# Kernel tuning notes

Measured on AMD Instinct MI355X. Metric: run time of the kernel, lower is better.

The kernel has to match this reference:

```python
import jax, jax.numpy as jnp
import numpy as np

UNITS = 32
SENSORY = 16
MOTOR = 3
ODE_UNFOLDS = 3
EPS = 1e-8


def setup_inputs() -> dict:
    key = jax.random.key(0)
    ks = jax.random.split(key, 16)
    B, T, D = 64, 512, 6
    return {
        "x": jax.random.normal(ks[0], (B, T, D), jnp.float32),
        "mean_us": jax.random.normal(ks[1], (1, 1, D), jnp.float32),
        "std_us": jnp.ones((1, 1, D), jnp.float32),
        "pre_w1": jax.random.normal(ks[2], (D, 32), jnp.float32) * 0.4,
        "pre_b1": jnp.zeros((32,), jnp.float32),
        "pre_w2": jax.random.normal(ks[3], (32, SENSORY), jnp.float32) * 0.18,
        "pre_b2": jnp.zeros((SENSORY,), jnp.float32),
        "input_w": jnp.ones((SENSORY,), jnp.float32),
        "input_b": jnp.zeros((SENSORY,), jnp.float32),
        "sensory_mu": jax.random.uniform(ks[4], (SENSORY, UNITS), jnp.float32),
        "sensory_sigma": jax.random.uniform(ks[5], (SENSORY, UNITS), jnp.float32),
        "sensory_w": jax.random.uniform(ks[6], (SENSORY, UNITS), jnp.float32),
        "sensory_erev": jax.random.normal(ks[7], (SENSORY, UNITS), jnp.float32),
        "mu": jax.random.uniform(ks[8], (UNITS, UNITS), jnp.float32),
        "sigma": jax.random.uniform(ks[9], (UNITS, UNITS), jnp.float32),
        "w": jax.random.uniform(ks[10], (UNITS, UNITS), jnp.float32),
        "erev": jax.random.normal(ks[11], (UNITS, UNITS), jnp.float32),
        "gleak": jax.random.uniform(ks[12], (UNITS,), jnp.float32),
        "vleak": jax.random.normal(ks[13], (UNITS,), jnp.float32),
        "cm": jax.random.uniform(ks[14], (UNITS,), jnp.float32) + 0.1,
        "output_w": jnp.ones((MOTOR,), jnp.float32),
        "output_b": jnp.zeros((MOTOR,), jnp.float32),
    }


def reference(x, mean_us, std_us, pre_w1, pre_b1, pre_w2, pre_b2,
              input_w, input_b, sensory_mu, sensory_sigma, sensory_w,
              sensory_erev, mu, sigma, w, erev, gleak, vleak, cm,
              output_w, output_b):
    B = x.shape[0]
    # normalize (broadcast of [1,1,6] stats == expand_as in torch)
    xn = (x - mean_us) / std_us
    # DgaPreNet: per-timestep MLP 6 -> 32 -> 16
    feat = jax.nn.gelu(jnp.einsum("btd,dh->bth", xn, pre_w1) + pre_b1)
    feat = jnp.einsum("bth,hs->bts", feat, pre_w2) + pre_b2  # [B,T,S]
    # LTC input mapping
    feat = feat * input_w + input_b
    # sensory synapse activations, precomputed for all timesteps
    s_act = sensory_w * jax.nn.sigmoid(sensory_sigma * (feat[..., None] - sensory_mu))  # [B,T,S,U]
    w_num_sens = jnp.einsum("btsu,su->btu", s_act, sensory_erev)  # [B,T,U]
    w_den_sens = s_act.sum(axis=2)                                # [B,T,U]
    cm_t = cm * ODE_UNFOLDS  # cm / (elapsed_time=1 / ode_unfolds)

    def step(v, inp):
        wns, wds = inp  # [B,U] each
        for _ in range(ODE_UNFOLDS):
            act = w * jax.nn.sigmoid(sigma * (v[:, :, None] - mu))  # [B,U_pre,U_post]
            w_num = jnp.einsum("bpu,pu->bu", act, erev) + wns
            w_den = act.sum(axis=1) + wds
            v = (cm_t * v + gleak * vleak + w_num) / (cm_t + gleak + w_den + EPS)
        out = v[:, :MOTOR] * output_w + output_b
        return v, out

    v0 = jnp.zeros((B, UNITS), x.dtype)
    _, outs = jax.lax.scan(step, v0,
                           (jnp.swapaxes(w_num_sens, 0, 1), jnp.swapaxes(w_den_sens, 0, 1)))
    outs = jnp.swapaxes(outs, 0, 1)  # [B,T,3]
    return outs * std_us[:, :, 0:MOTOR] + mean_us[:, :, 0:MOTOR]
```

## Files before the change

### kernel.cpp

```cpp
#include <hip/hip_runtime.h>

#define T_LEN 512
#define BATCH 64
#define LOG2E 1.4426950408889634f

typedef float v2f __attribute__((ext_vector_type(2)));

#if defined(__has_builtin)
#  if __has_builtin(__builtin_amdgcn_exp2f)
#    define EXP2F(x) __builtin_amdgcn_exp2f(x)
#  endif
#endif
#ifndef EXP2F
#  define EXP2F(x) __expf((x) * 0.6931471805599453f)
#endif

__device__ __forceinline__ float fast_sigmoid(float x) {
    return __builtin_amdgcn_rcpf(1.0f + __expf(-x));
}

__global__ __launch_bounds__(256, 1) void sensory_precompute_kernel(
    const float* __restrict__ x,
    const float* __restrict__ mean_us,
    const float* __restrict__ std_us,
    const float* __restrict__ pre_w1,
    const float* __restrict__ pre_b1,
    const float* __restrict__ pre_w2,
    const float* __restrict__ pre_b2,
    const float* __restrict__ input_w,
    const float* __restrict__ input_b,
    const float* __restrict__ s_mu,
    const float* __restrict__ s_sigma,
    const float* __restrict__ s_w,
    const float* __restrict__ s_erev,
    float* __restrict__ wnd_out,
    int total)
{
    const int idx = blockIdx.x * blockDim.x + threadIdx.x;
    if (idx >= total) return;

    const float* xp = x + (size_t)idx * 6;
    float xn[6];
    #pragma unroll
    for (int d = 0; d < 6; ++d)
        xn[d] = (xp[d] - mean_us[d]) / std_us[d];

    float f1[32];
    #pragma unroll
    for (int h = 0; h < 32; ++h) {
        float a = pre_b1[h];
        #pragma unroll
        for (int d = 0; d < 6; ++d)
            a = fmaf(xn[d], pre_w1[d * 32 + h], a);
        const float y2 = 1.5957691216057308f * fmaf(0.044715f * a * a, a, a);
        f1[h] = a * fast_sigmoid(y2);
    }

    float wn[32], wd[32];
    #pragma unroll
    for (int u = 0; u < 32; ++u) { wn[u] = 0.0f; wd[u] = 0.0f; }

    for (int s = 0; s < 16; ++s) {
        float a = pre_b2[s];
        #pragma unroll
        for (int h = 0; h < 32; ++h)
            a = fmaf(f1[h], pre_w2[h * 16 + s], a);
        const float fs = fmaf(a, input_w[s], input_b[s]);
        #pragma unroll
        for (int u = 0; u < 32; ++u) {
            const int o = s * 32 + u;
            const float sact =
                s_w[o] * fast_sigmoid(s_sigma[o] * (fs - s_mu[o]));
            wn[u] = fmaf(sact, s_erev[o], wn[u]);
            wd[u] += sact;
        }
    }

    float* wo = wnd_out + (size_t)idx * 64;
    #pragma unroll
    for (int u = 0; u < 32; ++u) {
        wo[u * 2]     = wn[u];
        wo[u * 2 + 1] = wd[u];
    }
}

__global__ __launch_bounds__(64, 1) void ltc_scan_kernel(
    const float* __restrict__ wnd_all,
    const float* __restrict__ mu,
    const float* __restrict__ sigma,
    const float* __restrict__ w,
    const float* __restrict__ erev,
    const float* __restrict__ gleak,
    const float* __restrict__ vleak,
    const float* __restrict__ cm,
    const float* __restrict__ output_w,
    const float* __restrict__ output_b,
    const float* __restrict__ mean_us,
    const float* __restrict__ std_us,
    float* __restrict__ out)
{
    const int b = blockIdx.x;
    const int lane = threadIdx.x;
    const int u = lane & 31;
    const int pbase = (lane >> 5) << 4;

    __shared__ float vbuf[64];

    v2f A2[8], B2[8], W2[8], WE2[8];
    #pragma unroll
    for (int i = 0; i < 16; ++i) {
        const int o = (pbase + i) * 32 + u;
        const float sg = sigma[o];
        const float ww = w[o];
        A2[i >> 1][i & 1]  = -sg * LOG2E;
        B2[i >> 1][i & 1]  = sg * mu[o] * LOG2E;
        W2[i >> 1][i & 1]  = ww;
        WE2[i >> 1][i & 1] = ww * erev[o];
    }
    const float cmt  = cm[u] * 3.0f;
    const float gl   = gleak[u];
    const float glvl = gl * vleak[u];

    float osc = 0.0f, osh = 0.0f;
    if (lane < 3) {
        const float sd = std_us[lane];
        osc = output_w[lane] * sd;
        osh = fmaf(output_b[lane], sd, mean_us[lane]);
    }

    const float* wnd_b = wnd_all + (size_t)b * T_LEN * 64 + u * 2;
    float* out_b = out + ((size_t)b * T_LEN) * 3;

    float v = 0.0f;
    vbuf[lane] = 0.0f;
    float2 wnd = *(const float2*)wnd_b;

    for (int t = 0; t < T_LEN; ++t) {
        float2 wnd_n = make_float2(0.0f, 0.0f);
        if (t + 1 < T_LEN)
            wnd_n = *(const float2*)(wnd_b + (size_t)(t + 1) * 64);

        #pragma unroll
        for (int k = 0; k < 3; ++k) {
            const float4* vb = (const float4*)(vbuf + pbase);
            const float4 q0 = vb[0], q1 = vb[1], q2 = vb[2], q3 = vb[3];
            v2f vp[8];
            vp[0] = (v2f){q0.x, q0.y}; vp[1] = (v2f){q0.z, q0.w};
            vp[2] = (v2f){q1.x, q1.y}; vp[3] = (v2f){q1.z, q1.w};
            vp[4] = (v2f){q2.x, q2.y}; vp[5] = (v2f){q2.z, q2.w};
            vp[6] = (v2f){q3.x, q3.y}; vp[7] = (v2f){q3.z, q3.w};

            v2f wna = (v2f){0.f, 0.f}, wnb = (v2f){0.f, 0.f};
            v2f wda = (v2f){0.f, 0.f}, wdb = (v2f){0.f, 0.f};
            #pragma unroll
            for (int j = 0; j < 8; ++j) {
                const v2f arg = A2[j] * vp[j] + B2[j];
                v2f e;
                e.x = EXP2F(arg.x);
                e.y = EXP2F(arg.y);
                const v2f d = e + 1.0f;
                v2f s;
                s.x = __builtin_amdgcn_rcpf(d.x);
                s.y = __builtin_amdgcn_rcpf(d.y);
                if (j & 1) { wnb = WE2[j] * s + wnb; wdb = W2[j] * s + wdb; }
                else       { wna = WE2[j] * s + wna; wda = W2[j] * s + wda; }
            }
            const v2f wn2 = wna + wnb;
            const v2f wd2 = wda + wdb;
            float wnum = wn2.x + wn2.y;
            float wden = wd2.x + wd2.y;
            wnum += __shfl_xor(wnum, 32, 64);
            wden += __shfl_xor(wden, 32, 64);

            const float num = fmaf(cmt, v, glvl + wnum + wnd.x);
            const float den = cmt + gl + wden + wnd.y + 1e-8f;
            v = num * __builtin_amdgcn_rcpf(den);
            vbuf[lane] = v;
        }

        if (lane < 3)
            out_b[t * 3 + lane] = fmaf(v, osc, osh);

        wnd = wnd_n;
    }
}

extern "C" void kernel_launch(void* const* d_in, const int* in_sizes, int n_in,
                              void* d_out, int out_size, void* d_ws, size_t ws_size,
                              hipStream_t stream) {
    const float* x        = (const float*)d_in[0];
    const float* mean_us  = (const float*)d_in[1];
    const float* std_us   = (const float*)d_in[2];
    const float* pre_w1   = (const float*)d_in[3];
    const float* pre_b1   = (const float*)d_in[4];
    const float* pre_w2   = (const float*)d_in[5];
    const float* pre_b2   = (const float*)d_in[6];
    const float* input_w  = (const float*)d_in[7];
    const float* input_b  = (const float*)d_in[8];
    const float* s_mu     = (const float*)d_in[9];
    const float* s_sigma  = (const float*)d_in[10];
    const float* s_w      = (const float*)d_in[11];
    const float* s_erev   = (const float*)d_in[12];
    const float* mu       = (const float*)d_in[13];
    const float* sigma    = (const float*)d_in[14];
    const float* w        = (const float*)d_in[15];
    const float* erev     = (const float*)d_in[16];
    const float* gleak    = (const float*)d_in[17];
    const float* vleak    = (const float*)d_in[18];
    const float* cm       = (const float*)d_in[19];
    const float* output_w = (const float*)d_in[20];
    const float* output_b = (const float*)d_in[21];

    const int total = BATCH * T_LEN;

    float* wnd = (float*)d_ws;

    sensory_precompute_kernel<<<(total + 255) / 256, 256, 0, stream>>>(
        x, mean_us, std_us, pre_w1, pre_b1, pre_w2, pre_b2,
        input_w, input_b, s_mu, s_sigma, s_w, s_erev,
        wnd, total);

    ltc_scan_kernel<<<BATCH, 64, 0, stream>>>(
        wnd, mu, sigma, w, erev, gleak, vleak, cm,
        output_w, output_b, mean_us, std_us, (float*)d_out);
}
```

Baseline: 592.8 us.

## Broadcast scan state with permlane/DPP cross-lane ops instead of LDS

Replaces the per-unfold LDS write and read of the voltage vector with a permlane16_swap followed by DPP xor shuffles. Each lane then gets its 16 presynaptic values in a permuted order, and the weight registers are permuted to match. The cross-half reduction moves from a shfl_xor (ds_bpermute) to permlane32_swap. A runtime self-test checks that the intrinsics behave as expected and falls back to the original LDS path if they do not. The goal is to shorten the serial latency of each recurrent step, at the cost of a duplicated loop body and an added startup check.

```diff
diff --git a/kernel.cpp b/kernel.cpp
--- a/kernel.cpp
+++ b/kernel.cpp
@@ -5,10 +5,17 @@
 #define LOG2E 1.4426950408889634f
 
 typedef float v2f __attribute__((ext_vector_type(2)));
-
-#if defined(__has_builtin)
+typedef unsigned u2i __attribute__((ext_vector_type(2)));
+
+#ifdef __has_builtin
 #  if __has_builtin(__builtin_amdgcn_exp2f)
 #    define EXP2F(x) __builtin_amdgcn_exp2f(x)
+#  endif
+#  if __has_builtin(__builtin_amdgcn_permlane32_swap)
+#    define HAVE_PL32 1
+#  endif
+#  if __has_builtin(__builtin_amdgcn_permlane16_swap)
+#    define HAVE_PL16 1
 #  endif
 #endif
 #ifndef EXP2F
@@ -17,6 +24,60 @@
 
 __device__ __forceinline__ float fast_sigmoid(float x) {
     return __builtin_amdgcn_rcpf(1.0f + __expf(-x));
+}
+
+__device__ __forceinline__ float pl32_sum(float x) {
+#ifdef HAVE_PL32
+    const unsigned xi = __builtin_bit_cast(unsigned, x);
+    const u2i r = __builtin_amdgcn_permlane32_swap(xi, xi, false, false);
+    return __builtin_bit_cast(float, r.x) + __builtin_bit_cast(float, r.y);
+#else
+    return x + __shfl_xor(x, 32, 64);
+#endif
+}
+
+template <int CTRL>
+__device__ __forceinline__ float dppf(float x) {
+    const int xi = __builtin_bit_cast(int, x);
+    const int r = __builtin_amdgcn_update_dpp(xi, xi, CTRL, 0xF, 0xF, true);
+    return __builtin_bit_cast(float, r);
+}
+#define DPP_XOR1  0xB1
+#define DPP_XOR2  0x4E
+#define DPP_XOR3  0x1B
+#define DPP_XOR7  0x141
+#define DPP_XOR15 0x140
+
+__device__ __forceinline__ void fast_vp(float v, int lane, float vp[16]) {
+    float vlo, vhi;
+#ifdef HAVE_PL16
+    {
+        const unsigned xi = __builtin_bit_cast(unsigned, v);
+        const u2i r = __builtin_amdgcn_permlane16_swap(xi, xi, false, false);
+        vlo = __builtin_bit_cast(float, r.x);
+        vhi = __builtin_bit_cast(float, r.y);
+    }
+#else
+    vlo = __shfl(v, lane & 15, 64);
+    vhi = __shfl(v, 16 + (lane & 15), 64);
+#endif
+    const float vs = (lane & 32) ? vhi : vlo;
+    vp[0]  = vs;
+    vp[1]  = dppf<DPP_XOR1>(vs);
+    vp[2]  = dppf<DPP_XOR2>(vs);
+    vp[3]  = dppf<DPP_XOR3>(vs);
+    vp[7]  = dppf<DPP_XOR7>(vp[0]);
+    vp[6]  = dppf<DPP_XOR7>(vp[1]);
+    vp[5]  = dppf<DPP_XOR7>(vp[2]);
+    vp[4]  = dppf<DPP_XOR7>(vp[3]);
+    vp[15] = dppf<DPP_XOR15>(vp[0]);
+    vp[14] = dppf<DPP_XOR15>(vp[1]);
+    vp[13] = dppf<DPP_XOR15>(vp[2]);
+    vp[12] = dppf<DPP_XOR15>(vp[3]);
+    vp[11] = dppf<DPP_XOR15>(vp[4]);
+    vp[10] = dppf<DPP_XOR15>(vp[5]);
+    vp[9]  = dppf<DPP_XOR15>(vp[6]);
+    vp[8]  = dppf<DPP_XOR15>(vp[7]);
 }
 
 __global__ __launch_bounds__(256, 1) void sensory_precompute_kernel(
@@ -102,20 +163,36 @@
     const int b = blockIdx.x;
     const int lane = threadIdx.x;
     const int u = lane & 31;
+    const int lx = lane & 15;
     const int pbase = (lane >> 5) << 4;
 
     __shared__ float vbuf[64];
 
+    bool ok = true;
+    {
+        const float tv = (float)(u * 8 + 3);
+        float tvp[16];
+        fast_vp(tv, lane, tvp);
+        #pragma unroll
+        for (int j = 0; j < 16; ++j)
+            ok = ok && (tvp[j] == (float)((pbase + (lx ^ j)) * 8 + 3));
+        const float tg = (float)(lane * 4 + 7);
+        const float ts = pl32_sum(tg);
+        ok = ok && (ts == (float)(lane * 4 + 7) + (float)((lane ^ 32) * 4 + 7));
+    }
+    const bool fast = (__ballot(ok) == 0xFFFFFFFFFFFFFFFFull);
+
     v2f A2[8], B2[8], W2[8], WE2[8];
     #pragma unroll
-    for (int i = 0; i < 16; ++i) {
-        const int o = (pbase + i) * 32 + u;
+    for (int j = 0; j < 16; ++j) {
+        const int p = pbase + (fast ? (lx ^ j) : j);
+        const int o = p * 32 + u;
         const float sg = sigma[o];
         const float ww = w[o];
-        A2[i >> 1][i & 1]  = -sg * LOG2E;
-        B2[i >> 1][i & 1]  = sg * mu[o] * LOG2E;
-        W2[i >> 1][i & 1]  = ww;
-        WE2[i >> 1][i & 1] = ww * erev[o];
+        A2[j >> 1][j & 1]  = -sg * LOG2E;
+        B2[j >> 1][j & 1]  = sg * mu[o] * LOG2E;
+        W2[j >> 1][j & 1]  = ww;
+        WE2[j >> 1][j & 1] = ww * erev[o];
     }
     const float cmt  = cm[u] * 3.0f;
     const float gl   = gleak[u];
@@ -135,53 +212,97 @@
     vbuf[lane] = 0.0f;
     float2 wnd = *(const float2*)wnd_b;
 
-    for (int t = 0; t < T_LEN; ++t) {
-        float2 wnd_n = make_float2(0.0f, 0.0f);
-        if (t + 1 < T_LEN)
-            wnd_n = *(const float2*)(wnd_b + (size_t)(t + 1) * 64);
-
-        #pragma unroll
-        for (int k = 0; k < 3; ++k) {
-            const float4* vb = (const float4*)(vbuf + pbase);
-            const float4 q0 = vb[0], q1 = vb[1], q2 = vb[2], q3 = vb[3];
-            v2f vp[8];
-            vp[0] = (v2f){q0.x, q0.y}; vp[1] = (v2f){q0.z, q0.w};
-            vp[2] = (v2f){q1.x, q1.y}; vp[3] = (v2f){q1.z, q1.w};
-            vp[4] = (v2f){q2.x, q2.y}; vp[5] = (v2f){q2.z, q2.w};
-            vp[6] = (v2f){q3.x, q3.y}; vp[7] = (v2f){q3.z, q3.w};
-
-            v2f wna = (v2f){0.f, 0.f}, wnb = (v2f){0.f, 0.f};
-            v2f wda = (v2f){0.f, 0.f}, wdb = (v2f){0.f, 0.f};
+    if (fast) {
+        for (int t = 0; t < T_LEN; ++t) {
+            float2 wnd_n = make_float2(0.0f, 0.0f);
+            if (t + 1 < T_LEN)
+                wnd_n = *(const float2*)(wnd_b + (size_t)(t + 1) * 64);
+
             #pragma unroll
-            for (int j = 0; j < 8; ++j) {
-                const v2f arg = A2[j] * vp[j] + B2[j];
-                v2f e;
-                e.x = EXP2F(arg.x);
-                e.y = EXP2F(arg.y);
-                const v2f d = e + 1.0f;
-                v2f s;
-                s.x = __builtin_amdgcn_rcpf(d.x);
-                s.y = __builtin_amdgcn_rcpf(d.y);
-                if (j & 1) { wnb = WE2[j] * s + wnb; wdb = W2[j] * s + wdb; }
-                else       { wna = WE2[j] * s + wna; wda = W2[j] * s + wda; }
+            for (int k = 0; k < 3; ++k) {
+                float vp[16];
+                fast_vp(v, lane, vp);
+
+                v2f wna = (v2f){0.f, 0.f}, wnb = (v2f){0.f, 0.f};
+                v2f wda = (v2f){0.f, 0.f}, wdb = (v2f){0.f, 0.f};
+                #pragma unroll
+                for (int j = 0; j < 8; ++j) {
+                    const v2f vv = (v2f){vp[2 * j], vp[2 * j + 1]};
+                    const v2f arg = A2[j] * vv + B2[j];
+                    v2f e;
+                    e.x = EXP2F(arg.x);
+                    e.y = EXP2F(arg.y);
+                    const v2f d = e + 1.0f;
+                    v2f s;
+                    s.x = __builtin_amdgcn_rcpf(d.x);
+                    s.y = __builtin_amdgcn_rcpf(d.y);
+                    if (j & 1) { wnb = WE2[j] * s + wnb; wdb = W2[j] * s + wdb; }
+                    else       { wna = WE2[j] * s + wna; wda = W2[j] * s + wda; }
+                }
+                const v2f wn2 = wna + wnb;
+                const v2f wd2 = wda + wdb;
+                const float wnum = pl32_sum(wn2.x + wn2.y);
+                const float wden = pl32_sum(wd2.x + wd2.y);
+
+                const float num = fmaf(cmt, v, glvl + wnum + wnd.x);
+                const float den = cmt + gl + wden + wnd.y + 1e-8f;
+                v = num * __builtin_amdgcn_rcpf(den);
             }
-            const v2f wn2 = wna + wnb;
-            const v2f wd2 = wda + wdb;
-            float wnum = wn2.x + wn2.y;
-            float wden = wd2.x + wd2.y;
-            wnum += __shfl_xor(wnum, 32, 64);
-            wden += __shfl_xor(wden, 32, 64);
-
-            const float num = fmaf(cmt, v, glvl + wnum + wnd.x);
-            const float den = cmt + gl + wden + wnd.y + 1e-8f;
-            v = num * __builtin_amdgcn_rcpf(den);
-            vbuf[lane] = v;
+
+            if (lane < 3)
+                out_b[t * 3 + lane] = fmaf(v, osc, osh);
+
+            wnd = wnd_n;
         }
-
-        if (lane < 3)
-            out_b[t * 3 + lane] = fmaf(v, osc, osh);
-
-        wnd = wnd_n;
+    } else {
+        for (int t = 0; t < T_LEN; ++t) {
+            float2 wnd_n = make_float2(0.0f, 0.0f);
+            if (t + 1 < T_LEN)
+                wnd_n = *(const float2*)(wnd_b + (size_t)(t + 1) * 64);
+
+            #pragma unroll
+            for (int k = 0; k < 3; ++k) {
+                const float4* vb = (const float4*)(vbuf + pbase);
+                const float4 q0 = vb[0], q1 = vb[1], q2 = vb[2], q3 = vb[3];
+                v2f vp[8];
+                vp[0] = (v2f){q0.x, q0.y}; vp[1] = (v2f){q0.z, q0.w};
+                vp[2] = (v2f){q1.x, q1.y}; vp[3] = (v2f){q1.z, q1.w};
+                vp[4] = (v2f){q2.x, q2.y}; vp[5] = (v2f){q2.z, q2.w};
+                vp[6] = (v2f){q3.x, q3.y}; vp[7] = (v2f){q3.z, q3.w};
+
+                v2f wna = (v2f){0.f, 0.f}, wnb = (v2f){0.f, 0.f};
+                v2f wda = (v2f){0.f, 0.f}, wdb = (v2f){0.f, 0.f};
+                #pragma unroll
+                for (int j = 0; j < 8; ++j) {
+                    const v2f arg = A2[j] * vp[j] + B2[j];
+                    v2f e;
+                    e.x = EXP2F(arg.x);
+                    e.y = EXP2F(arg.y);
+                    const v2f d = e + 1.0f;
+                    v2f s;
+                    s.x = __builtin_amdgcn_rcpf(d.x);
+                    s.y = __builtin_amdgcn_rcpf(d.y);
+                    if (j & 1) { wnb = WE2[j] * s + wnb; wdb = W2[j] * s + wdb; }
+                    else       { wna = WE2[j] * s + wna; wda = W2[j] * s + wda; }
+                }
+                const v2f wn2 = wna + wnb;
+                const v2f wd2 = wda + wdb;
+                float wnum = wn2.x + wn2.y;
+                float wden = wd2.x + wd2.y;
+                wnum += __shfl_xor(wnum, 32, 64);
+                wden += __shfl_xor(wden, 32, 64);
+
+                const float num = fmaf(cmt, v, glvl + wnum + wnd.x);
+                const float den = cmt + gl + wden + wnd.y + 1e-8f;
+                v = num * __builtin_amdgcn_rcpf(den);
+                vbuf[lane] = v;
+            }
+
+            if (lane < 3)
+                out_b[t * 3 + lane] = fmaf(v, osc, osh);
+
+            wnd = wnd_n;
+        }
     }
 }
 
```

Measured after the change: 533.4 us. -10.0%, faster.
